# Performance work log

Measured on AMD Instinct MI355X. Metric: run time of the kernel, lower is better.

## Reference

```python
import jax, jax.numpy as jnp
import numpy as np

EPS = 1e-6
ROPE_THETA = 1000000.0
SPAN_LENGTHS = [700, 300, 600, 448]
L, D, H, HK, DH, FF = 2, 2048, 16, 8, 128, 8192


def _rmsnorm(x, w):
    var = jnp.mean(jnp.square(x), axis=-1, keepdims=True)
    return x * jax.lax.rsqrt(var + EPS) * w


def _rotate_half(x):
    x1, x2 = jnp.split(x, 2, axis=-1)
    return jnp.concatenate([-x2, x1], axis=-1)


def setup_inputs() -> dict:
    key = jax.random.key(0)
    ks = jax.random.split(key, 8)
    s = 0.02  # init scale
    seg = np.repeat(np.arange(len(SPAN_LENGTHS), dtype=np.int32), SPAN_LENGTHS)
    pos = np.concatenate([np.arange(n, dtype=np.int32) for n in SPAN_LENGTHS])
    T = seg.shape[0]
    return {
        "hidden_states": jax.random.normal(ks[0], (T, D), jnp.float32),
        "ln1_w": jnp.ones((L, D), jnp.float32),
        "ln2_w": jnp.ones((L, D), jnp.float32),
        "wq": jax.random.normal(ks[1], (L, D, H * DH), jnp.float32) * s,
        "wk": jax.random.normal(ks[2], (L, D, HK * DH), jnp.float32) * s,
        "wv": jax.random.normal(ks[3], (L, D, HK * DH), jnp.float32) * s,
        "wo": jax.random.normal(ks[4], (L, H * DH, D), jnp.float32) * s,
        "qn_w": jnp.ones((L, DH), jnp.float32),
        "kn_w": jnp.ones((L, DH), jnp.float32),
        "wg": jax.random.normal(ks[5], (L, D, FF), jnp.float32) * s,
        "wu": jax.random.normal(ks[6], (L, D, FF), jnp.float32) * s,
        "wd": jax.random.normal(ks[7], (L, FF, D), jnp.float32) * s,
        "final_norm_w": jnp.ones((D,), jnp.float32),
        "segment_ids": jnp.asarray(seg),
        "position_ids": jnp.asarray(pos),
    }


def reference(hidden_states, ln1_w, ln2_w, wq, wk, wv, wo, qn_w, kn_w, wg, wu, wd, final_norm_w, segment_ids, position_ids):
    T = hidden_states.shape[0]
    # rotary tables from per-request positions (positions reset per span)
    inv_freq = 1.0 / (ROPE_THETA ** (jnp.arange(0, DH, 2, dtype=jnp.float32) / DH))
    freqs = position_ids.astype(jnp.float32)[:, None] * inv_freq  # [T, DH/2]
    emb = jnp.concatenate([freqs, freqs], axis=-1)                # [T, DH]
    cos = jnp.cos(emb)[:, None, :]
    sin = jnp.sin(emb)[:, None, :]
    # ragged causal mask: attend only within the same request span, causally
    tok = jnp.arange(T)
    mask = (segment_ids[:, None] == segment_ids[None, :]) & (tok[:, None] >= tok[None, :])
    neg = jnp.finfo(hidden_states.dtype).min
    scale = 1.0 / np.sqrt(DH)

    x = hidden_states
    for l in range(L):
        h = _rmsnorm(x, ln1_w[l])
        q = (h @ wq[l]).reshape(T, H, DH)
        k = (h @ wk[l]).reshape(T, HK, DH)
        v = (h @ wv[l]).reshape(T, HK, DH)
        q = _rmsnorm(q, qn_w[l])  # Qwen3 per-head q/k RMSNorm
        k = _rmsnorm(k, kn_w[l])
        q = q * cos + _rotate_half(q) * sin
        k = k * cos + _rotate_half(k) * sin
        rep = H // HK  # GQA
        k = jnp.repeat(k, rep, axis=1)
        v = jnp.repeat(v, rep, axis=1)
        scores = jnp.einsum('thd,shd->hts', q, k) * scale  # [H, T, T]
        scores = jnp.where(mask[None], scores, neg)
        attn = jax.nn.softmax(scores, axis=-1)
        o = jnp.einsum('hts,shd->thd', attn, v).reshape(T, H * DH)
        x = x + o @ wo[l]
        h = _rmsnorm(x, ln2_w[l])
        x = x + (jax.nn.silu(h @ wg[l]) * (h @ wu[l])) @ wd[l]
    return _rmsnorm(x, final_norm_w)
```

## Files before the change

### kernel.cpp

```cpp
#include <hip/hip_runtime.h>
#include <stdint.h>

#define T_SEQ 2048
#define DMODEL 2048
#define NH 16
#define NKV 8
#define DHEAD 128
#define DFF 8192

typedef float f32x4 __attribute__((ext_vector_type(4)));
typedef float f32x2 __attribute__((ext_vector_type(2)));
typedef __bf16 bf16x8 __attribute__((ext_vector_type(8)));
typedef unsigned short ushort8 __attribute__((ext_vector_type(8)));
typedef unsigned short ushort_t;

typedef __attribute__((address_space(1))) void gvoid;
typedef __attribute__((address_space(3))) void lvoid;

__device__ inline unsigned short f2bf(float f) {
  unsigned int u = __float_as_uint(f);
  u += 0x7fffu + ((u >> 16) & 1u);
  return (unsigned short)(u >> 16);
}
__device__ inline float bf2f(unsigned short h) {
  return __uint_as_float(((unsigned int)h) << 16);
}

__device__ inline void gload_lds16(const void* g, void* l) {
  __builtin_amdgcn_global_load_lds((gvoid*)g, (lvoid*)l, 16, 0, 0);
}

template <typename TIN>
__global__ __launch_bounds__(256) void k_transpose_bf16(const TIN* __restrict__ in,
                                                        ushort_t* __restrict__ out,
                                                        int R, int C, int rmode) {
  __shared__ float tile[64 * 72];
  int tid = threadIdx.x;
  int r0 = blockIdx.y * 64, c0 = blockIdx.x * 64;
  int rl = tid >> 4;
  int cc = tid & 15;
#pragma unroll
  for (int i = 0; i < 4; ++i) {
    int row = rl + i * 16;
    const TIN* src = in + (size_t)(r0 + row) * C + c0 + cc * 4;
    float v0, v1, v2, v3;
    if constexpr (sizeof(TIN) == 4) {
      f32x4 v = *(const f32x4*)src;
      v0 = v.x; v1 = v.y; v2 = v.z; v3 = v.w;
    } else {
      ushort4 v = *(const ushort4*)src;
      v0 = bf2f(v.x); v1 = bf2f(v.y); v2 = bf2f(v.z); v3 = bf2f(v.w);
    }
    int chunk = cc ^ (row & 15);
    f32x4 t = {v0, v1, v2, v3};
    *(f32x4*)&tile[row * 72 + chunk * 4] = t;
  }
  __syncthreads();
#pragma unroll
  for (int i = 0; i < 4; ++i) {
    int nrow = rl + i * 16;
    int k4 = cc * 4;
    ushort4 o;
    {
      int k = k4 + 0;
      o.x = f2bf(tile[k * 72 + (((nrow >> 2) ^ (k & 15)) << 2) + (nrow & 3)]);
      k = k4 + 1;
      o.y = f2bf(tile[k * 72 + (((nrow >> 2) ^ (k & 15)) << 2) + (nrow & 3)]);
      k = k4 + 2;
      o.z = f2bf(tile[k * 72 + (((nrow >> 2) ^ (k & 15)) << 2) + (nrow & 3)]);
      k = k4 + 3;
      o.w = f2bf(tile[k * 72 + (((nrow >> 2) ^ (k & 15)) << 2) + (nrow & 3)]);
    }
    int n = c0 + nrow;
    int orow = n;
    if (rmode == 1) orow = ((n >> 4) << 5) + (n & 15);
    else if (rmode == 2) orow = ((n >> 4) << 5) + 16 + (n & 15);
    *(ushort4*)(out + (size_t)orow * R + r0 + k4) = o;
  }
}

template <int BF16OUT>
__global__ __launch_bounds__(256) void k_rmsnorm(const float* __restrict__ X,
                                                 const float* __restrict__ W,
                                                 void* __restrict__ OUT) {
  int row = blockIdx.x, tid = threadIdx.x;
  const float* xr = X + (size_t)row * DMODEL;
  f32x4 x0 = *(const f32x4*)(xr + tid * 4);
  f32x4 x1 = *(const f32x4*)(xr + 1024 + tid * 4);
  float ss = x0.x * x0.x + x0.y * x0.y + x0.z * x0.z + x0.w * x0.w +
             x1.x * x1.x + x1.y * x1.y + x1.z * x1.z + x1.w * x1.w;
#pragma unroll
  for (int o = 1; o < 64; o <<= 1) ss += __shfl_xor(ss, o, 64);
  __shared__ float red[4];
  int w = tid >> 6;
  if ((tid & 63) == 0) red[w] = ss;
  __syncthreads();
  float tot = red[0] + red[1] + red[2] + red[3];
  float sc = rsqrtf(tot / (float)DMODEL + 1e-6f);
  f32x4 w0 = *(const f32x4*)(W + tid * 4);
  f32x4 w1 = *(const f32x4*)(W + 1024 + tid * 4);
  if constexpr (BF16OUT) {
    ushort_t* o = (ushort_t*)OUT + (size_t)row * DMODEL;
    ushort4 a, b;
    a.x = f2bf(x0.x * sc * w0.x); a.y = f2bf(x0.y * sc * w0.y);
    a.z = f2bf(x0.z * sc * w0.z); a.w = f2bf(x0.w * sc * w0.w);
    b.x = f2bf(x1.x * sc * w1.x); b.y = f2bf(x1.y * sc * w1.y);
    b.z = f2bf(x1.z * sc * w1.z); b.w = f2bf(x1.w * sc * w1.w);
    *(ushort4*)(o + tid * 4) = a;
    *(ushort4*)(o + 1024 + tid * 4) = b;
  } else {
    float* o = (float*)OUT + (size_t)row * DMODEL;
    f32x4 a = {x0.x * sc * w0.x, x0.y * sc * w0.y, x0.z * sc * w0.z, x0.w * sc * w0.w};
    f32x4 b = {x1.x * sc * w1.x, x1.y * sc * w1.y, x1.z * sc * w1.z, x1.w * sc * w1.w};
    *(f32x4*)(o + tid * 4) = a;
    *(f32x4*)(o + 1024 + tid * 4) = b;
  }
}

template <int NZ, int WRITEH>
__global__ __launch_bounds__(512) void k_redln(const ushort_t* __restrict__ P,
                                               const float* __restrict__ RES,
                                               const float* __restrict__ W,
                                               float* __restrict__ OUT,
                                               ushort_t* __restrict__ HB) {
  int row = blockIdx.x, tid = threadIdx.x;
  size_t base = (size_t)row * DMODEL + tid * 4;
  f32x4 v = *(const f32x4*)(RES + base);
#pragma unroll
  for (int z = 0; z < NZ; ++z) {
    ushort4 t = *(const ushort4*)(P + (size_t)z * T_SEQ * DMODEL + base);
    v.x += bf2f(t.x); v.y += bf2f(t.y); v.z += bf2f(t.z); v.w += bf2f(t.w);
  }
  if constexpr (WRITEH != 2) *(f32x4*)(OUT + base) = v;
  if constexpr (WRITEH >= 1) {
    float ss = v.x * v.x + v.y * v.y + v.z * v.z + v.w * v.w;
#pragma unroll
    for (int o = 1; o < 64; o <<= 1) ss += __shfl_xor(ss, o, 64);
    __shared__ float red[8];
    if ((tid & 63) == 0) red[tid >> 6] = ss;
    __syncthreads();
    float tot = 0.f;
#pragma unroll
    for (int i = 0; i < 8; ++i) tot += red[i];
    float sc = rsqrtf(tot / (float)DMODEL + 1e-6f);
    f32x4 wv = *(const f32x4*)(W + tid * 4);
    if constexpr (WRITEH == 1) {
      ushort4 h;
      h.x = f2bf(v.x * sc * wv.x); h.y = f2bf(v.y * sc * wv.y);
      h.z = f2bf(v.z * sc * wv.z); h.w = f2bf(v.w * sc * wv.w);
      *(ushort4*)(HB + base) = h;
    } else {
      f32x4 o = {v.x * sc * wv.x, v.y * sc * wv.y, v.z * sc * wv.z, v.w * sc * wv.w};
      *(f32x4*)(OUT + base) = o;
    }
  }
}

#define EPI_STOREB 3
#define EPI_GLU 5

#define LOADB(dst, bs, rbase)                                                  \
  {                                                                            \
    _Pragma("unroll") for (int ks = 0; ks < 2; ++ks)                           \
        _Pragma("unroll") for (int ni = 0; ni < 2; ++ni)                       \
            dst[ks][ni] = *(const bf16x8*)((bs) +                              \
                (((rbase) + ni * 16 + lr) << 6) +                              \
                ((((ks << 2) + lg) ^ (lr & 7)) << 3));                         \
  }

#define MFMA_Q(q, B)                                                           \
  {                                                                            \
    _Pragma("unroll") for (int ks = 0; ks < 2; ++ks)                           \
        _Pragma("unroll") for (int mi = 0; mi < 4; ++mi)                       \
            _Pragma("unroll") for (int ni = 0; ni < 2; ++ni)                   \
                acc[mi][(q) * 2 + ni] =                                        \
                    __builtin_amdgcn_mfma_f32_16x16x32_bf16(                   \
                        af[ks][mi], B[ks][ni], acc[mi][(q) * 2 + ni], 0, 0, 0); \
  }

template <int LAST>
__device__ __forceinline__ void g256_iter(
    const ushort_t* __restrict__ as, const ushort_t* __restrict__ bsA,
    const ushort_t* __restrict__ bsB, ushort_t* __restrict__ nA,
    ushort_t* __restrict__ nB, const ushort_t* __restrict__ an,
    const ushort_t* __restrict__ bn, size_t rs, int slds, int lr, int lg,
    f32x4 (&acc)[4][8]) {
  bf16x8 af[2][4], b0[2][2], b1[2][2];
#pragma unroll
  for (int ks = 0; ks < 2; ++ks)
#pragma unroll
    for (int mi = 0; mi < 4; ++mi)
      af[ks][mi] = *(const bf16x8*)(as + ((mi * 16 + lr) << 6) +
                                    ((((ks << 2) + lg) ^ (lr & 7)) << 3));
  LOADB(b0, bsA, 0);
  if constexpr (!LAST) {
    gload_lds16(an, nA + slds);
    gload_lds16(an + rs, nA + 4096 + slds);
    gload_lds16(an + 2 * rs, nA + 8192 + slds);
    gload_lds16(an + 3 * rs, nA + 12288 + slds);
    gload_lds16(bn, nB + slds);
    gload_lds16(bn + rs, nB + 4096 + slds);
    gload_lds16(bn + 2 * rs, nB + 8192 + slds);
    gload_lds16(bn + 3 * rs, nB + 12288 + slds);
  }
  LOADB(b1, bsA, 32);
  asm volatile("s_waitcnt lgkmcnt(4)" ::: "memory");
  __builtin_amdgcn_sched_barrier(0);
  __builtin_amdgcn_s_setprio(1);
  MFMA_Q(0, b0);
  __builtin_amdgcn_s_setprio(0);
  LOADB(b0, bsB, 0);
  asm volatile("s_waitcnt lgkmcnt(4)" ::: "memory");
  __builtin_amdgcn_sched_barrier(0);
  __builtin_amdgcn_s_setprio(1);
  MFMA_Q(1, b1);
  __builtin_amdgcn_s_setprio(0);
  LOADB(b1, bsB, 32);
  asm volatile("s_waitcnt lgkmcnt(4)" ::: "memory");
  __builtin_amdgcn_sched_barrier(0);
  __builtin_amdgcn_s_setprio(1);
  MFMA_Q(2, b0);
  __builtin_amdgcn_s_setprio(0);
  asm volatile("s_waitcnt lgkmcnt(0)" ::: "memory");
  __builtin_amdgcn_sched_barrier(0);
  __builtin_amdgcn_s_setprio(1);
  MFMA_Q(3, b1);
  __builtin_amdgcn_s_setprio(0);
  if constexpr (!LAST) {
    asm volatile("s_waitcnt vmcnt(0)" ::: "memory");
    __builtin_amdgcn_s_barrier();
  }
}

template <int EPI>
__global__ __launch_bounds__(512, 2) void k_gemm256(
    const ushort_t* __restrict__ A, const ushort_t* __restrict__ BT,
    ushort_t* __restrict__ CB, int N, int Kstride, int Kc, size_t zoff) {
  __shared__ ushort_t lds[65536];
  const int tid = threadIdx.x;
  const int l = tid & 63, wid = tid >> 6;
  const int wm = wid >> 1, wn = wid & 1;
  const int lr = l & 15, lg = l >> 4;
  const int gx = gridDim.x;
  const int nwg = gx * gridDim.y;
  const int bid = blockIdx.x + gx * blockIdx.y;
  const int chunk = nwg >> 3;
  const int x = bid & 7;
  const int local = bid >> 3;
  const int cn = chunk >> 2;
  const int ncx = gx / cn;
  const int m0 = ((x / ncx) * 4 + local / cn) * 256;
  const int n0 = ((x % ncx) * cn + local % cn) * 256;
  const int z = blockIdx.z;
  const int NT = Kc >> 6;

  A += (size_t)z * Kc;
  BT += (size_t)z * Kc;
  CB += (size_t)z * zoff;

  const int srow = tid >> 3;
  const int scs = (tid & 7) ^ (srow & 7);
  const size_t sgoff = (size_t)srow * Kstride + scs * 8;
  const int slds = wid * 512;

  const ushort_t* ga = A + (size_t)m0 * Kstride + sgoff;
  const ushort_t* gb = BT + (size_t)n0 * Kstride + sgoff;
  const size_t rs = (size_t)64 * Kstride;

  f32x4 acc[4][8] = {};

  ushort_t* Ab0 = lds;
  ushort_t* Bb0 = lds + 16384;
  ushort_t* Ab1 = lds + 32768;
  ushort_t* Bb1 = lds + 49152;

  gload_lds16(ga, Ab0 + slds);
  gload_lds16(ga + rs, Ab0 + 4096 + slds);
  gload_lds16(ga + 2 * rs, Ab0 + 8192 + slds);
  gload_lds16(ga + 3 * rs, Ab0 + 12288 + slds);
  gload_lds16(gb, Bb0 + slds);
  gload_lds16(gb + rs, Bb0 + 4096 + slds);
  gload_lds16(gb + 2 * rs, Bb0 + 8192 + slds);
  gload_lds16(gb + 3 * rs, Bb0 + 12288 + slds);
  asm volatile("s_waitcnt vmcnt(0)" ::: "memory");
  __builtin_amdgcn_s_barrier();

  for (int kt = 0; kt < NT - 1; ++kt) {
    const int d = kt & 1;
    const ushort_t* as = (d ? Ab1 : Ab0) + wm * 4096;
    const ushort_t* bsA = (d ? Bb1 : Bb0) + (wn * 2) * 4096;
    ushort_t* nA = d ? Ab0 : Ab1;
    ushort_t* nB = d ? Bb0 : Bb1;
    g256_iter<0>(as, bsA, bsA + 4096, nA, nB, ga + (size_t)(kt + 1) * 64,
                 gb + (size_t)(kt + 1) * 64, rs, slds, lr, lg, acc);
  }
  {
    const int d = (NT - 1) & 1;
    const ushort_t* as = (d ? Ab1 : Ab0) + wm * 4096;
    const ushort_t* bsA = (d ? Bb1 : Bb0) + (wn * 2) * 4096;
    g256_iter<1>(as, bsA, bsA + 4096, nullptr, nullptr, nullptr, nullptr, rs,
                 slds, lr, lg, acc);
  }

  if constexpr (EPI == EPI_GLU) {
#pragma unroll
    for (int mi = 0; mi < 4; ++mi)
#pragma unroll
      for (int ci = 0; ci < 8; ci += 2)
#pragma unroll
        for (int rr = 0; rr < 4; ++rr) {
          int m = m0 + wm * 64 + mi * 16 + lg * 4 + rr;
          int nblk = n0 + wn * 128 + ci * 16;
          int col = ((nblk >> 5) << 4) + lr;
          float gv = acc[mi][ci][rr];
          float uv = acc[mi][ci + 1][rr];
          float s = gv / (1.f + __expf(-gv));
          CB[(size_t)m * 8192 + col] = f2bf(s * uv);
        }
  } else {
#pragma unroll
    for (int mi = 0; mi < 4; ++mi)
#pragma unroll
      for (int ci = 0; ci < 8; ++ci)
#pragma unroll
        for (int rr = 0; rr < 4; ++rr) {
          int m = m0 + wm * 64 + mi * 16 + lg * 4 + rr;
          int n = n0 + wn * 128 + ci * 16 + lr;
          CB[(size_t)m * N + n] = f2bf(acc[mi][ci][rr]);
        }
  }
}

__global__ __launch_bounds__(64) void k_ropetab(const int* __restrict__ POS,
                                                float* __restrict__ CS,
                                                float* __restrict__ SN) {
  int t = blockIdx.x, d = threadIdx.x;
  const float K2 = 19.931568569324174f / 64.f;
  float ang = (float)POS[t] * exp2f(-(float)d * K2);
  CS[t * 64 + d] = cosf(ang);
  SN[t * 64 + d] = sinf(ang);
}

__global__ __launch_bounds__(256) void k_qkv_post(const ushort_t* __restrict__ Q0,
                                                  const ushort_t* __restrict__ Q1,
                                                  const float* __restrict__ QNW,
                                                  const float* __restrict__ KNW,
                                                  const float* __restrict__ CS,
                                                  const float* __restrict__ SN,
                                                  ushort_t* __restrict__ Qb,
                                                  ushort_t* __restrict__ Kb,
                                                  ushort_t* __restrict__ Vb) {
  int t = blockIdx.x, tid = threadIdx.x;
  int slot = tid >> 3, sub = tid & 7;
  int d0 = sub * 16;
  size_t off = (size_t)t * 4096 + slot * 128 + d0;
  ushort8 a0 = *(const ushort8*)(Q0 + off);
  ushort8 a1 = *(const ushort8*)(Q0 + off + 8);
  ushort8 b0 = *(const ushort8*)(Q1 + off);
  ushort8 b1 = *(const ushort8*)(Q1 + off + 8);
  float v[16];
#pragma unroll
  for (int e = 0; e < 8; ++e) {
    v[e] = bf2f(a0[e]) + bf2f(b0[e]);
    v[8 + e] = bf2f(a1[e]) + bf2f(b1[e]);
  }
  float ss = 0.f;
#pragma unroll
  for (int e = 0; e < 16; ++e) ss += v[e] * v[e];
#pragma unroll
  for (int o = 1; o < 8; o <<= 1) ss += __shfl_xor(ss, o, 64);
  ushort_t* dst;
  if (slot < 16) dst = Qb + (size_t)t * 2048 + slot * 128 + d0;
  else if (slot < 24) dst = Kb + (size_t)t * 1024 + (slot - 16) * 128 + d0;
  else dst = Vb + (size_t)t * 1024 + (slot - 24) * 128 + d0;
  ushort8 o0, o1;
  if (slot < 24) {
    float sc = rsqrtf(ss * (1.f / 128.f) + 1e-6f);
    const float* nw = (slot < 16) ? QNW : KNW;
    float w[16], cs[16], sn[16];
    int ci = t * 64 + (d0 & 63);
#pragma unroll
    for (int i = 0; i < 4; ++i) {
      *(f32x4*)&w[i * 4] = *(const f32x4*)(nw + d0 + i * 4);
      *(f32x4*)&cs[i * 4] = *(const f32x4*)(CS + ci + i * 4);
      *(f32x4*)&sn[i * 4] = *(const f32x4*)(SN + ci + i * 4);
    }
#pragma unroll
    for (int e = 0; e < 16; ++e) v[e] = v[e] * sc * w[e];
    float o[16];
#pragma unroll
    for (int e = 0; e < 16; ++e) {
      float p = __shfl_xor(v[e], 4, 64);
      float rot = (sub < 4) ? -p : p;
      o[e] = v[e] * cs[e] + rot * sn[e];
    }
#pragma unroll
    for (int e = 0; e < 8; ++e) {
      o0[e] = f2bf(o[e]);
      o1[e] = f2bf(o[8 + e]);
    }
  } else {
#pragma unroll
    for (int e = 0; e < 8; ++e) {
      o0[e] = f2bf(v[e]);
      o1[e] = f2bf(v[8 + e]);
    }
  }
  *(ushort8*)dst = o0;
  *(ushort8*)(dst + 8) = o1;
}

__global__ __launch_bounds__(64) void k_flash(const ushort_t* __restrict__ Qb,
                                              const ushort_t* __restrict__ Kb,
                                              const ushort_t* __restrict__ VT,
                                              const int* __restrict__ SEG,
                                              ushort_t* __restrict__ Ob) {
  __shared__ ushort_t Pl[16 * 40];
  int l = threadIdx.x;
  int qt = blockIdx.x, h = blockIdx.y;
  int q0 = qt * 16;
  int lr = l & 15, lg = l >> 4;
  int kvh = h >> 1;
  bf16x8 qf[4];
  {
    const bf16x8* qv = (const bf16x8*)(Qb + (size_t)(q0 + lr) * 2048 + h * 128);
#pragma unroll
    for (int kk = 0; kk < 4; ++kk) qf[kk] = qv[kk * 4 + lg];
  }
  int segq[4];
#pragma unroll
  for (int r = 0; r < 4; ++r) segq[r] = SEG[q0 + lg * 4 + r];
  int target = SEG[q0];
  int lo = 0, hi = q0;
  while (lo < hi) {
    int mid = (lo + hi) >> 1;
    if (SEG[mid] < target) lo = mid + 1; else hi = mid;
  }
  int s_start = lo & ~31;
  float m_run[4], l_run[4];
  f32x4 acc[8] = {};
#pragma unroll
  for (int r = 0; r < 4; ++r) { m_run[r] = -1e30f; l_run[r] = 0.f; }
  const float scale = 0.08838834764831845f;
  for (int s0 = s_start; s0 < q0 + 16; s0 += 32) {
    int sa = s0 + lr, sb = s0 + 16 + lr;
    int sac = min(sa, T_SEQ - 1), sbc = min(sb, T_SEQ - 1);
    bf16x8 vfr[8];
    int sbase = min(s0 + lg * 8, T_SEQ - 8);
#pragma unroll
    for (int c = 0; c < 8; ++c)
      vfr[c] = *(const bf16x8*)(VT + (size_t)(kvh * 128 + c * 16 + lr) * T_SEQ + sbase);
    f32x4 SA = {}, SB = {};
    const bf16x8* ka = (const bf16x8*)(Kb + (size_t)sac * 1024 + kvh * 128);
    const bf16x8* kb_ = (const bf16x8*)(Kb + (size_t)sbc * 1024 + kvh * 128);
    __builtin_amdgcn_s_setprio(1);
#pragma unroll
    for (int kk = 0; kk < 4; ++kk) {
      SA = __builtin_amdgcn_mfma_f32_16x16x32_bf16(qf[kk], ka[kk * 4 + lg], SA, 0, 0, 0);
      SB = __builtin_amdgcn_mfma_f32_16x16x32_bf16(qf[kk], kb_[kk * 4 + lg], SB, 0, 0, 0);
    }
    __builtin_amdgcn_s_setprio(0);
    int sga = SEG[sac], sgb = SEG[sbc];
    float al[4], pA[4], pB[4];
#pragma unroll
    for (int r = 0; r < 4; ++r) {
      int qrow = q0 + lg * 4 + r;
      float xa = (sa <= qrow && sga == segq[r]) ? SA[r] * scale : -1e30f;
      float xb = (sb <= qrow && sgb == segq[r]) ? SB[r] * scale : -1e30f;
      float mx = fmaxf(xa, xb);
#pragma unroll
      for (int o = 1; o < 16; o <<= 1) mx = fmaxf(mx, __shfl_xor(mx, o, 64));
      float nm = fmaxf(m_run[r], mx);
      float ea = __expf(xa - nm), eb = __expf(xb - nm);
      float rs = ea + eb;
#pragma unroll
      for (int o = 1; o < 16; o <<= 1) rs += __shfl_xor(rs, o, 64);
      al[r] = __expf(m_run[r] - nm);
      l_run[r] = l_run[r] * al[r] + rs;
      m_run[r] = nm;
      pA[r] = ea;
      pB[r] = eb;
    }
#pragma unroll
    for (int c = 0; c < 8; ++c)
#pragma unroll
      for (int r = 0; r < 4; ++r) acc[c][r] *= al[r];
#pragma unroll
    for (int r = 0; r < 4; ++r) {
      Pl[(lg * 4 + r) * 40 + lr] = f2bf(pA[r]);
      Pl[(lg * 4 + r) * 40 + 16 + lr] = f2bf(pB[r]);
    }
    asm volatile("s_waitcnt lgkmcnt(0)" ::: "memory");
    bf16x8 pa = *(const bf16x8*)&Pl[lr * 40 + lg * 8];
    __builtin_amdgcn_s_setprio(1);
#pragma unroll
    for (int c = 0; c < 8; ++c)
      acc[c] = __builtin_amdgcn_mfma_f32_16x16x32_bf16(pa, vfr[c], acc[c], 0, 0, 0);
    __builtin_amdgcn_s_setprio(0);
  }
#pragma unroll
  for (int c = 0; c < 8; ++c)
#pragma unroll
    for (int r = 0; r < 4; ++r) {
      float ov = acc[c][r] / l_run[r];
      Ob[(size_t)(q0 + lg * 4 + r) * 2048 + h * 128 + c * 16 + lr] = f2bf(ov);
    }
}

extern "C" void kernel_launch(void* const* d_in, const int* in_sizes, int n_in,
                              void* d_out, int out_size, void* d_ws, size_t ws_size,
                              hipStream_t stream) {
  const float* hidden = (const float*)d_in[0];
  const float* ln1 = (const float*)d_in[1];
  const float* ln2 = (const float*)d_in[2];
  const float* wq = (const float*)d_in[3];
  const float* wk = (const float*)d_in[4];
  const float* wv = (const float*)d_in[5];
  const float* wo = (const float*)d_in[6];
  const float* qnw = (const float*)d_in[7];
  const float* knw = (const float*)d_in[8];
  const float* wg = (const float*)d_in[9];
  const float* wu = (const float*)d_in[10];
  const float* wd = (const float*)d_in[11];
  const float* fnw = (const float*)d_in[12];
  const int* seg = (const int*)d_in[13];
  const int* pos = (const int*)d_in[14];
  float* out = (float*)d_out;

  char* ws = (char*)d_ws;
  size_t off = 0;
  auto alloc = [&](size_t bytes) {
    char* p = ws + off;
    off += (bytes + 255) & ~(size_t)255;
    return p;
  };
  ushort_t* wT = (ushort_t*)alloc((size_t)2 * DFF * DMODEL * 2);
  ushort_t* hbuf = (ushort_t*)alloc((size_t)T_SEQ * DMODEL * 2);
  ushort_t* qb = (ushort_t*)alloc((size_t)T_SEQ * 2048 * 2);
  ushort_t* kb = (ushort_t*)alloc((size_t)T_SEQ * 1024 * 2);
  ushort_t* vb = (ushort_t*)alloc((size_t)T_SEQ * 1024 * 2);
  ushort_t* vT = (ushort_t*)alloc((size_t)T_SEQ * 1024 * 2);
  ushort_t* ob = (ushort_t*)alloc((size_t)T_SEQ * 2048 * 2);
  ushort_t* qkvp = (ushort_t*)alloc((size_t)2 * T_SEQ * 4096 * 2);
  ushort_t* pbuf = (ushort_t*)alloc((size_t)4 * T_SEQ * DMODEL * 2);
  ushort_t* mbuf = (ushort_t*)alloc((size_t)T_SEQ * DFF * 2);
  float* cstab = (float*)alloc((size_t)T_SEQ * 64 * 4);
  float* sntab = (float*)alloc((size_t)T_SEQ * 64 * 4);
  (void)ws_size; (void)in_sizes; (void)n_in; (void)out_size;

  dim3 b256(256), b64(64), b512(512);
  k_ropetab<<<T_SEQ, b64, 0, stream>>>(pos, cstab, sntab);
  k_rmsnorm<1><<<T_SEQ, b256, 0, stream>>>(hidden, ln1, hbuf);

  for (int lyr = 0; lyr < 2; ++lyr) {
    const float* xsrc = (lyr == 0) ? hidden : out;

    const float* wql = wq + (size_t)lyr * DMODEL * 2048;
    const float* wkl = wk + (size_t)lyr * DMODEL * 1024;
    const float* wvl = wv + (size_t)lyr * DMODEL * 1024;
    k_transpose_bf16<float><<<dim3(32, 32), b256, 0, stream>>>(wql, wT, 2048, 2048, 0);
    k_transpose_bf16<float><<<dim3(16, 32), b256, 0, stream>>>(wkl, wT + (size_t)2048 * 2048, 2048, 1024, 0);
    k_transpose_bf16<float><<<dim3(16, 32), b256, 0, stream>>>(wvl, wT + (size_t)3072 * 2048, 2048, 1024, 0);
    k_gemm256<EPI_STOREB><<<dim3(16, 8, 2), b512, 0, stream>>>(
        hbuf, wT, qkvp, 4096, 2048, 1024, (size_t)2048 * 4096);
    k_qkv_post<<<T_SEQ, b256, 0, stream>>>(qkvp, qkvp + (size_t)2048 * 4096,
                                           qnw + (size_t)lyr * 128, knw + (size_t)lyr * 128,
                                           cstab, sntab, qb, kb, vb);
    k_transpose_bf16<ushort_t><<<dim3(16, 32), b256, 0, stream>>>(vb, vT, 2048, 1024, 0);
    k_flash<<<dim3(T_SEQ / 16, NH), b64, 0, stream>>>(qb, kb, vT, seg, ob);

    const float* wol = wo + (size_t)lyr * 2048 * DMODEL;
    k_transpose_bf16<float><<<dim3(32, 32), b256, 0, stream>>>(wol, wT, 2048, 2048, 0);
    k_gemm256<EPI_STOREB><<<dim3(8, 8, 4), b512, 0, stream>>>(
        ob, wT, pbuf, 2048, 2048, 512, (size_t)2048 * 2048);
    k_redln<4, 1><<<T_SEQ, b512, 0, stream>>>(pbuf, xsrc,
                                              ln2 + (size_t)lyr * DMODEL, out, hbuf);

    const float* wgl = wg + (size_t)lyr * DMODEL * DFF;
    const float* wul = wu + (size_t)lyr * DMODEL * DFF;
    const float* wdl = wd + (size_t)lyr * DFF * DMODEL;
    k_transpose_bf16<float><<<dim3(128, 32), b256, 0, stream>>>(wgl, wT, 2048, 8192, 1);
    k_transpose_bf16<float><<<dim3(128, 32), b256, 0, stream>>>(wul, wT, 2048, 8192, 2);
    k_gemm256<EPI_GLU><<<dim3(64, 8, 1), b512, 0, stream>>>(
        hbuf, wT, mbuf, 16384, 2048, 2048, 0);
    k_transpose_bf16<float><<<dim3(32, 128), b256, 0, stream>>>(wdl, wT, 8192, 2048, 0);
    k_gemm256<EPI_STOREB><<<dim3(8, 8, 4), b512, 0, stream>>>(
        mbuf, wT, pbuf, 2048, 8192, 2048, (size_t)2048 * 2048);
    if (lyr == 0) {
      k_redln<4, 1><<<T_SEQ, b512, 0, stream>>>(pbuf, out, ln1 + DMODEL, out, hbuf);
    } else {
      k_redln<4, 2><<<T_SEQ, b512, 0, stream>>>(pbuf, out, fnw, out, nullptr);
    }
  }
}
```

Before: 906.1 us.

## Process both GQA query heads per flash block to share K/V loads

```diff
diff --git a/kernel.cpp b/kernel.cpp
--- a/kernel.cpp
+++ b/kernel.cpp
@@ -415,17 +415,20 @@
                                               const ushort_t* __restrict__ VT,
                                               const int* __restrict__ SEG,
                                               ushort_t* __restrict__ Ob) {
-  __shared__ ushort_t Pl[16 * 40];
+  __shared__ ushort_t Pl[2][16 * 40];
   int l = threadIdx.x;
-  int qt = blockIdx.x, h = blockIdx.y;
+  int qt = blockIdx.x, kvh = blockIdx.y;
   int q0 = qt * 16;
   int lr = l & 15, lg = l >> 4;
-  int kvh = h >> 1;
-  bf16x8 qf[4];
+  int h0 = kvh * 2;
+  bf16x8 qf0[4], qf1[4];
   {
-    const bf16x8* qv = (const bf16x8*)(Qb + (size_t)(q0 + lr) * 2048 + h * 128);
-#pragma unroll
-    for (int kk = 0; kk < 4; ++kk) qf[kk] = qv[kk * 4 + lg];
+    const bf16x8* qv = (const bf16x8*)(Qb + (size_t)(q0 + lr) * 2048 + h0 * 128);
+#pragma unroll
+    for (int kk = 0; kk < 4; ++kk) {
+      qf0[kk] = qv[kk * 4 + lg];
+      qf1[kk] = qv[16 + kk * 4 + lg];
+    }
   }
   int segq[4];
 #pragma unroll
@@ -437,10 +440,12 @@
     if (SEG[mid] < target) lo = mid + 1; else hi = mid;
   }
   int s_start = lo & ~31;
-  float m_run[4], l_run[4];
-  f32x4 acc[8] = {};
-#pragma unroll
-  for (int r = 0; r < 4; ++r) { m_run[r] = -1e30f; l_run[r] = 0.f; }
+  float mr[2][4], lrun[2][4];
+  f32x4 acc[2][8] = {};
+#pragma unroll
+  for (int h = 0; h < 2; ++h)
+#pragma unroll
+    for (int r = 0; r < 4; ++r) { mr[h][r] = -1e30f; lrun[h][r] = 0.f; }
   const float scale = 0.08838834764831845f;
   for (int s0 = s_start; s0 < q0 + 16; s0 += 32) {
     int sa = s0 + lr, sb = s0 + 16 + lr;
@@ -450,61 +455,73 @@
 #pragma unroll
     for (int c = 0; c < 8; ++c)
       vfr[c] = *(const bf16x8*)(VT + (size_t)(kvh * 128 + c * 16 + lr) * T_SEQ + sbase);
-    f32x4 SA = {}, SB = {};
+    f32x4 SA0 = {}, SB0 = {}, SA1 = {}, SB1 = {};
     const bf16x8* ka = (const bf16x8*)(Kb + (size_t)sac * 1024 + kvh * 128);
     const bf16x8* kb_ = (const bf16x8*)(Kb + (size_t)sbc * 1024 + kvh * 128);
     __builtin_amdgcn_s_setprio(1);
 #pragma unroll
     for (int kk = 0; kk < 4; ++kk) {
-      SA = __builtin_amdgcn_mfma_f32_16x16x32_bf16(qf[kk], ka[kk * 4 + lg], SA, 0, 0, 0);
-      SB = __builtin_amdgcn_mfma_f32_16x16x32_bf16(qf[kk], kb_[kk * 4 + lg], SB, 0, 0, 0);
+      bf16x8 kaf = ka[kk * 4 + lg];
+      bf16x8 kbf = kb_[kk * 4 + lg];
+      SA0 = __builtin_amdgcn_mfma_f32_16x16x32_bf16(qf0[kk], kaf, SA0, 0, 0, 0);
+      SB0 = __builtin_amdgcn_mfma_f32_16x16x32_bf16(qf0[kk], kbf, SB0, 0, 0, 0);
+      SA1 = __builtin_amdgcn_mfma_f32_16x16x32_bf16(qf1[kk], kaf, SA1, 0, 0, 0);
+      SB1 = __builtin_amdgcn_mfma_f32_16x16x32_bf16(qf1[kk], kbf, SB1, 0, 0, 0);
     }
     __builtin_amdgcn_s_setprio(0);
     int sga = SEG[sac], sgb = SEG[sbc];
-    float al[4], pA[4], pB[4];
+    bool mAv[4], mBv[4];
 #pragma unroll
     for (int r = 0; r < 4; ++r) {
       int qrow = q0 + lg * 4 + r;
-      float xa = (sa <= qrow && sga == segq[r]) ? SA[r] * scale : -1e30f;
-      float xb = (sb <= qrow && sgb == segq[r]) ? SB[r] * scale : -1e30f;
-      float mx = fmaxf(xa, xb);
-#pragma unroll
-      for (int o = 1; o < 16; o <<= 1) mx = fmaxf(mx, __shfl_xor(mx, o, 64));
-      float nm = fmaxf(m_run[r], mx);
-      float ea = __expf(xa - nm), eb = __expf(xb - nm);
-      float rs = ea + eb;
-#pragma unroll
-      for (int o = 1; o < 16; o <<= 1) rs += __shfl_xor(rs, o, 64);
-      al[r] = __expf(m_run[r] - nm);
-      l_run[r] = l_run[r] * al[r] + rs;
-      m_run[r] = nm;
-      pA[r] = ea;
-      pB[r] = eb;
-    }
+      mAv[r] = (sa <= qrow) && (sga == segq[r]);
+      mBv[r] = (sb <= qrow) && (sgb == segq[r]);
+    }
+#pragma unroll
+    for (int h = 0; h < 2; ++h) {
+#pragma unroll
+      for (int r = 0; r < 4; ++r) {
+        float sva = (h ? SA1[r] : SA0[r]);
+        float svb = (h ? SB1[r] : SB0[r]);
+        float xa = mAv[r] ? sva * scale : -1e30f;
+        float xb = mBv[r] ? svb * scale : -1e30f;
+        float mx = fmaxf(xa, xb);
+#pragma unroll
+        for (int o = 1; o < 16; o <<= 1) mx = fmaxf(mx, __shfl_xor(mx, o, 64));
+        float nm = fmaxf(mr[h][r], mx);
+        float ea = __expf(xa - nm), eb = __expf(xb - nm);
+        float rsum = ea + eb;
+#pragma unroll
+        for (int o = 1; o < 16; o <<= 1) rsum += __shfl_xor(rsum, o, 64);
+        float al = __expf(mr[h][r] - nm);
+        lrun[h][r] = lrun[h][r] * al + rsum;
+        mr[h][r] = nm;
+#pragma unroll
+        for (int c = 0; c < 8; ++c) acc[h][c][r] *= al;
+        Pl[h][(lg * 4 + r) * 40 + lr] = f2bf(ea);
+        Pl[h][(lg * 4 + r) * 40 + 16 + lr] = f2bf(eb);
+      }
+    }
+    asm volatile("s_waitcnt lgkmcnt(0)" ::: "memory");
+    bf16x8 pa0 = *(const bf16x8*)&Pl[0][lr * 40 + lg * 8];
+    bf16x8 pa1 = *(const bf16x8*)&Pl[1][lr * 40 + lg * 8];
+    __builtin_amdgcn_s_setprio(1);
+#pragma unroll
+    for (int c = 0; c < 8; ++c) {
+      acc[0][c] = __builtin_amdgcn_mfma_f32_16x16x32_bf16(pa0, vfr[c], acc[0][c], 0, 0, 0);
+      acc[1][c] = __builtin_amdgcn_mfma_f32_16x16x32_bf16(pa1, vfr[c], acc[1][c], 0, 0, 0);
+    }
+    __builtin_amdgcn_s_setprio(0);
+  }
+#pragma unroll
+  for (int h = 0; h < 2; ++h)
 #pragma unroll
     for (int c = 0; c < 8; ++c)
 #pragma unroll
-      for (int r = 0; r < 4; ++r) acc[c][r] *= al[r];
-#pragma unroll
-    for (int r = 0; r < 4; ++r) {
-      Pl[(lg * 4 + r) * 40 + lr] = f2bf(pA[r]);
-      Pl[(lg * 4 + r) * 40 + 16 + lr] = f2bf(pB[r]);
-    }
-    asm volatile("s_waitcnt lgkmcnt(0)" ::: "memory");
-    bf16x8 pa = *(const bf16x8*)&Pl[lr * 40 + lg * 8];
-    __builtin_amdgcn_s_setprio(1);
-#pragma unroll
-    for (int c = 0; c < 8; ++c)
-      acc[c] = __builtin_amdgcn_mfma_f32_16x16x32_bf16(pa, vfr[c], acc[c], 0, 0, 0);
-    __builtin_amdgcn_s_setprio(0);
-  }
-#pragma unroll
-  for (int c = 0; c < 8; ++c)
-#pragma unroll
-    for (int r = 0; r < 4; ++r) {
-      float ov = acc[c][r] / l_run[r];
-      Ob[(size_t)(q0 + lg * 4 + r) * 2048 + h * 128 + c * 16 + lr] = f2bf(ov);
-    }
+      for (int r = 0; r < 4; ++r) {
+        float ov = acc[h][c][r] / lrun[h][r];
+        Ob[(size_t)(q0 + lg * 4 + r) * 2048 + (h0 + h) * 128 + c * 16 + lr] = f2bf(ov);
+      }
 }
 
 extern "C" void kernel_launch(void* const* d_in, const int* in_sizes, int n_in,
@@ -567,7 +584,7 @@
                                            qnw + (size_t)lyr * 128, knw + (size_t)lyr * 128,
                                            cstab, sntab, qb, kb, vb);
     k_transpose_bf16<ushort_t><<<dim3(16, 32), b256, 0, stream>>>(vb, vT, 2048, 1024, 0);
-    k_flash<<<dim3(T_SEQ / 16, NH), b64, 0, stream>>>(qb, kb, vT, seg, ob);
+    k_flash<<<dim3(T_SEQ / 16, NKV), b64, 0, stream>>>(qb, kb, vT, seg, ob);
 
     const float* wol = wo + (size_t)lyr * 2048 * DMODEL;
     k_transpose_bf16<float><<<dim3(32, 32), b256, 0, stream>>>(wol, wT, 2048, 2048, 0);
```

Measured after the change: 871.3 us. 1.04x faster.
